# Optimization experiments

Hardware: AMD Instinct MI355X
Metric: run time of the kernel (lower is better)

Reference implementation:

```python
import jax, jax.numpy as jnp
import numpy as np

B, T, C, H = 2, 2048, 1024, 16
DH = C // H  # 64


def setup_inputs() -> dict:
    key = jax.random.key(0)
    ks = jax.random.split(key, 8)
    scale = 1.0 / np.sqrt(C)
    x = jax.random.normal(ks[0], (B, T, C), dtype=jnp.float32)
    mask = jax.random.randint(ks[1], (B, T), 0, 2, dtype=jnp.int32)
    Wq = jax.random.normal(ks[2], (C, C), dtype=jnp.float32) * scale
    bq = jnp.zeros((C,), dtype=jnp.float32)
    Wk = jax.random.normal(ks[3], (C, C), dtype=jnp.float32) * scale
    bk = jnp.zeros((C,), dtype=jnp.float32)
    Wv = jax.random.normal(ks[4], (C, C), dtype=jnp.float32) * scale
    bv = jnp.zeros((C,), dtype=jnp.float32)
    return {"x": x, "Wq": Wq, "bq": bq, "Wk": Wk, "bk": bk, "Wv": Wv, "bv": bv, "mask": mask}


def reference(x, Wq, bq, Wk, bk, Wv, bv, mask):
    # q/k/v projections: [B,T,C] -> [B,H,T,DH]
    def proj(W, b):
        return (x @ W + b).reshape(B, T, H, DH).transpose(0, 2, 1, 3)

    q = proj(Wq, bq)
    k = proj(Wk, bk)
    v = proj(Wv, bv)

    att = jnp.einsum("bhqd,bhkd->bhqk", q, k) * (1.0 / np.sqrt(DH))

    # outer-product padding mask: square_mask[b,q,k] = mask[b,q]*mask[b,k]
    m = mask.astype(jnp.float32)
    square_mask = m[:, :, None] * m[:, None, :]           # [B,T,T]
    sm = (square_mask != 0)[:, None, :, :]                 # [B,1,T,T]
    att = jnp.where(sm, att, -jnp.inf)

    # rows that are fully masked (query token padded) -> softmax gives NaN
    # in torch; torch then zeros the NaNs. Replicate with a safe softmax.
    row_valid = (mask != 0)[:, None, :, None]              # [B,1,T,1]
    att_safe = jnp.where(row_valid, att, 0.0)
    att = jax.nn.softmax(att_safe, axis=-1)
    att = jnp.where(row_valid, att, 0.0)
    # attn_pdrop = 0.0 -> dropout is identity

    y = jnp.einsum("bhqk,bhkd->bhqd", att, v)              # [B,H,T,DH]
    y = y.transpose(0, 2, 1, 3).reshape(B, T, C)
    return y
```

## Files before the change

### kernel.cpp

```cpp
#include <hip/hip_runtime.h>

#define B_ 2
#define T_ 2048
#define C_ 1024
#define H_ 16
#define DH_ 64

typedef __attribute__((ext_vector_type(8))) _Float16 half8;
typedef __attribute__((ext_vector_type(4))) _Float16 half4;
typedef __attribute__((ext_vector_type(2))) __fp16 fp16x2;
typedef __attribute__((ext_vector_type(4))) float f32x4;
typedef __attribute__((ext_vector_type(16))) float f32x16;

__device__ __forceinline__ unsigned short f2h(float f) {
    union { _Float16 h; unsigned short u; } cv; cv.h = (_Float16)f; return cv.u;
}
__device__ __forceinline__ unsigned pk2(float a, float b) {
    union { fp16x2 h; unsigned u; } cv;
    cv.h = __builtin_amdgcn_cvt_pkrtz(a, b);
    return cv.u;
}
__device__ __forceinline__ void plswap(unsigned &a, unsigned &b) {
    asm volatile("v_permlane32_swap_b32 %0, %1" : "+v"(a), "+v"(b));
}

__device__ __forceinline__ void gll16(const void* g, void* l) {
    __builtin_amdgcn_global_load_lds(
        (const __attribute__((address_space(1))) void*)g,
        (__attribute__((address_space(3))) void*)l, 16, 0, 0);
}

__global__ __launch_bounds__(256) void prep_kernel(
    const float* __restrict__ x, unsigned short* __restrict__ xf,
    const int* __restrict__ mask, unsigned short* __restrict__ mb,
    const float* __restrict__ Wq, const float* __restrict__ Wk,
    const float* __restrict__ Wv, unsigned short* __restrict__ wt)
{
    __shared__ float tile[32][33];
    const int tid = threadIdx.x;

    if (blockIdx.x < 2048) {
        const size_t idx8 = ((size_t)blockIdx.x * 256 + tid) * 8;
        float4 v0 = *(const float4*)(x + idx8);
        float4 v1 = *(const float4*)(x + idx8 + 4);
        float f[8] = {v0.x, v0.y, v0.z, v0.w, v1.x, v1.y, v1.z, v1.w};
        unsigned short h[8];
#pragma unroll
        for (int i = 0; i < 8; i++) h[i] = f2h(f[i]);
        *(uint4*)(xf + idx8) = *(const uint4*)h;

        if (blockIdx.x == 0) {
#pragma unroll
            for (int j = 0; j < 16; j++) {
                int i = tid * 16 + j;
                mb[i] = (mask[i] != 0) ? (unsigned short)0x3C00 : (unsigned short)0;
            }
        }
    } else {
        const int idx = blockIdx.x - 2048;
        const int z   = idx >> 10;
        const int rem = idx & 1023;
        const int n0  = (rem & 31) * 32;
        const int k0  = (rem >> 5) * 32;
        const float* __restrict__ W = (z == 0) ? Wq : (z == 1) ? Wk : Wv;
        unsigned short* __restrict__ wtz = wt + (size_t)z * C_ * C_;
        const int tx = tid & 31;
        const int ty = tid >> 5;
#pragma unroll
        for (int j = 0; j < 4; j++)
            tile[ty + j * 8][tx] = W[(size_t)(k0 + ty + j * 8) * C_ + n0 + tx];
        __syncthreads();
#pragma unroll
        for (int j = 0; j < 4; j++)
            wtz[(size_t)(n0 + ty + j * 8) * C_ + k0 + tx] = f2h(tile[tx][ty + j * 8]);
    }
}

__global__ __launch_bounds__(256) void qkv_mfma_kernel(
    const unsigned short* __restrict__ xf, const unsigned short* __restrict__ wt,
    const float* __restrict__ bq, const float* __restrict__ bk,
    const float* __restrict__ bv, const int* __restrict__ maskp,
    unsigned short* __restrict__ qb, unsigned short* __restrict__ kb,
    unsigned short* __restrict__ vt)
{
    __shared__ unsigned short sX[128 * 64];
    __shared__ unsigned short sW[128 * 64];

    const int z = blockIdx.z;
    const float* __restrict__ bias = (z == 0) ? bq : (z == 1) ? bk : bv;
    const unsigned short* __restrict__ wtz = wt + (size_t)z * C_ * C_;

    const int tok0 = blockIdx.x * 128;
    const int col0 = blockIdx.y * 128;
    const int wv    = threadIdx.x >> 6;
    const int lane  = threadIdx.x & 63;
    const int l15   = lane & 15;
    const int quad  = lane >> 4;
    const int l7    = l15 & 7;
    const int wm    = wv >> 1;
    const int wn    = wv & 1;
    const int lrow8 = lane >> 3;
    const int gch   = (lane & 7) ^ lrow8;

    f32x4 acc[4][4];
#pragma unroll
    for (int i = 0; i < 4; i++)
#pragma unroll
        for (int j = 0; j < 4; j++) acc[i][j] = (f32x4){0.f, 0.f, 0.f, 0.f};

    int aoff[4][2], boff[4][2];
#pragma unroll
    for (int i = 0; i < 4; i++)
#pragma unroll
        for (int s = 0; s < 2; s++) {
            aoff[i][s] = (wm * 64 + i * 16 + l15) * 64 + (((s * 4 + quad) ^ l7) * 8);
            boff[i][s] = (wn * 64 + i * 16 + l15) * 64 + (((s * 4 + quad) ^ l7) * 8);
        }

    const unsigned short* Abuf = (z < 2) ? sX : sW;
    const unsigned short* Bbuf = (z < 2) ? sW : sX;

    for (int k0 = 0; k0 < C_; k0 += 64) {
        __syncthreads();
#pragma unroll
        for (int s = 0; s < 8; ++s) {
            int g    = (s << 2) + wv;
            int tsel = g >> 4;
            int r0   = (g & 15) << 3;
            const unsigned short* src = tsel ? wtz : xf;
            unsigned short*       dst = tsel ? sW  : sX;
            int rowg = tsel ? col0 : tok0;
            gll16(src + (size_t)(rowg + r0 + lrow8) * C_ + k0 + gch * 8,
                  dst + r0 * 64);
        }
        __syncthreads();

        half8 af[4][2], bf_[4][2];
#pragma unroll
        for (int i = 0; i < 4; i++)
#pragma unroll
            for (int s = 0; s < 2; s++) {
                af[i][s]  = *(const half8*)&Abuf[aoff[i][s]];
                bf_[i][s] = *(const half8*)&Bbuf[boff[i][s]];
            }
#pragma unroll
        for (int s = 0; s < 2; s++)
#pragma unroll
            for (int j = 0; j < 4; j++)
#pragma unroll
                for (int i = 0; i < 4; i++)
                    acc[i][j] = __builtin_amdgcn_mfma_f32_16x16x32_f16(
                        af[i][s], bf_[j][s], acc[i][j], 0, 0, 0);
    }

    if (z == 0) {
#pragma unroll
        for (int j = 0; j < 4; j++) {
            int col = col0 + wn * 64 + j * 16 + l15;
            int h = col >> 6, d = col & 63;
            float bs = bias[col];
#pragma unroll
            for (int i = 0; i < 4; i++) {
#pragma unroll
                for (int r = 0; r < 4; r++) {
                    int tok = tok0 + wm * 64 + i * 16 + quad * 4 + r;
                    int bidx = tok >> 11, t = tok & (T_ - 1);
                    qb[((size_t)(bidx * H_ + h) * T_ + t) * DH_ + d] =
                        f2h((acc[i][j][r] + bs) * 0.18033688011112042f);
                }
            }
        }
    } else if (z == 1) {
#pragma unroll
        for (int j = 0; j < 4; j++) {
            int col = col0 + wn * 64 + j * 16 + l15;
            int h = col >> 6, d = col & 63;
            float bs = bias[col];
#pragma unroll
            for (int i = 0; i < 4; i++) {
#pragma unroll
                for (int r = 0; r < 4; r++) {
                    int tok = tok0 + wm * 64 + i * 16 + quad * 4 + r;
                    int bidx = tok >> 11, t = tok & (T_ - 1);
                    kb[((size_t)(bidx * H_ + h) * T_ + t) * DH_ + d] =
                        f2h(acc[i][j][r] + bs);
                }
            }
        }
    } else {
        float mv4[4]; int bidx4[4], t4[4];
#pragma unroll
        for (int j = 0; j < 4; j++) {
            int tok = tok0 + wn * 64 + j * 16 + l15;
            bidx4[j] = tok >> 11; t4[j] = tok & (T_ - 1);
            mv4[j] = (maskp[bidx4[j] * T_ + t4[j]] != 0) ? 1.f : 0.f;
        }
#pragma unroll
        for (int i = 0; i < 4; i++) {
#pragma unroll
            for (int r = 0; r < 4; r++) {
                int col = col0 + wm * 64 + i * 16 + quad * 4 + r;
                int h = col >> 6, d = col & 63;
                float bs = bias[col];
#pragma unroll
                for (int j = 0; j < 4; j++) {
                    vt[((size_t)(bidx4[j] * H_ + h) * DH_ + d) * T_ + t4[j]] =
                        f2h((acc[i][j][r] + bs) * mv4[j]);
                }
            }
        }
    }
}

__global__ __launch_bounds__(256, 2) void attn_mfma_kernel(
    const unsigned short* __restrict__ qb,
    const unsigned short* __restrict__ kb,
    const unsigned short* __restrict__ vt,
    const int* __restrict__ mask,
    const unsigned short* __restrict__ mb,
    float* __restrict__ out)
{
    __shared__ unsigned short Ks[2][64 * 64];
    __shared__ unsigned short Vs[2][64 * 64];

    const int bh   = blockIdx.x;
    const int b    = bh >> 4;
    const int h    = bh & 15;
    const int wv   = threadIdx.x >> 6;
    const int lane = threadIdx.x & 63;
    const int l31  = lane & 31;
    const int hi   = lane >> 5;
    const int l7b  = l31 & 7;
    const int q0w  = blockIdx.y * 128 + wv * 32;

    const unsigned short* kbh = kb + (size_t)bh * T_ * DH_;
    const unsigned short* vbh = vt + (size_t)bh * DH_ * T_;
    const unsigned short* mbb = mb + b * T_;
    const int* __restrict__ mrow = mask + b * T_;

    half8 qf[4];
#pragma unroll
    for (int m = 0; m < 4; ++m)
        qf[m] = *(const half8*)(qb + ((size_t)bh * T_ + q0w + l31) * DH_
                                + m * 16 + hi * 8);

    f32x16 o0, o1, lacc;
#pragma unroll
    for (int r = 0; r < 16; ++r) { o0[r] = 0.f; o1[r] = 0.f; lacc[r] = 0.f; }

    const int lrow = lane >> 3;
    const int gch  = (lane & 7) ^ lrow;

#pragma unroll
    for (int s = 0; s < 4; ++s) {
        int j  = (wv << 2) + s;
        int rb = j & 7;
        if (j < 8) gll16(kbh + (size_t)(rb * 8 + lrow) * DH_ + gch * 8, &Ks[0][rb * 512]);
        else       gll16(vbh + (size_t)(rb * 8 + lrow) * T_  + gch * 8, &Vs[0][rb * 512]);
    }

    for (int kt = 0; kt < 32; ++kt) {
        const int cur   = kt & 1;
        const int kbase = kt * 64;
        __syncthreads();

        if (kt < 31) {
            const int nb = kbase + 64;
#pragma unroll
            for (int s = 0; s < 4; ++s) {
                int j  = (wv << 2) + s;
                int rb = j & 7;
                if (j < 8) gll16(kbh + (size_t)(nb + rb * 8 + lrow) * DH_ + gch * 8,
                                 &Ks[cur ^ 1][rb * 512]);
                else       gll16(vbh + (size_t)(rb * 8 + lrow) * T_ + nb + gch * 8,
                                 &Vs[cur ^ 1][rb * 512]);
            }
        }

        const unsigned short* Kc = &Ks[cur][0];
        const unsigned short* Vc = &Vs[cur][0];

        half8 bm[4];
#pragma unroll
        for (int c = 0; c < 4; ++c)
            bm[c] = *(const half8*)(mbb + kbase + c * 16 + hi * 8);

        half8 pa[4];
#pragma unroll
        for (int st = 0; st < 2; ++st) {
            f32x16 sa;
#pragma unroll
            for (int r = 0; r < 16; ++r) sa[r] = 0.f;
#pragma unroll
            for (int m = 0; m < 4; ++m) {
                half8 kf = *(const half8*)(Kc + (st * 32 + l31) * 64
                                           + (((m * 2 + hi) ^ l7b) * 8));
                sa = __builtin_amdgcn_mfma_f32_32x32x16_f16(kf, qf[m], sa, 0, 0, 0);
            }
            float p[16];
#pragma unroll
            for (int r = 0; r < 16; ++r) p[r] = __builtin_amdgcn_exp2f(sa[r]);
#pragma unroll
            for (int kh = 0; kh < 2; ++kh) {
                unsigned w0 = pk2(p[kh * 8 + 0], p[kh * 8 + 1]);
                unsigned w2 = pk2(p[kh * 8 + 4], p[kh * 8 + 5]);
                unsigned w1 = pk2(p[kh * 8 + 2], p[kh * 8 + 3]);
                unsigned w3 = pk2(p[kh * 8 + 6], p[kh * 8 + 7]);
                plswap(w0, w2);
                plswap(w1, w3);
                union { unsigned u[4]; half8 hh; } cv;
                cv.u[0] = w0; cv.u[1] = w1; cv.u[2] = w2; cv.u[3] = w3;
                pa[st * 2 + kh] = cv.hh;
            }
        }

#pragma unroll
        for (int c = 0; c < 4; ++c)
            lacc = __builtin_amdgcn_mfma_f32_32x32x16_f16(pa[c], bm[c], lacc, 0, 0, 0);

#pragma unroll
        for (int c = 0; c < 4; ++c) {
            half8 v0 = *(const half8*)(Vc + (l31) * 64      + (((c * 2 + hi) ^ l7b) * 8));
            half8 v1 = *(const half8*)(Vc + (32 + l31) * 64 + (((c * 2 + hi) ^ l7b) * 8));
            o0 = __builtin_amdgcn_mfma_f32_32x32x16_f16(pa[c], v0, o0, 0, 0, 0);
            o1 = __builtin_amdgcn_mfma_f32_32x32x16_f16(pa[c], v1, o1, 0, 0, 0);
        }
    }

#pragma unroll
    for (int r = 0; r < 16; ++r) {
        int q = q0w + (r & 3) + 8 * (r >> 2) + 4 * hi;
        float lv = lacc[r];
        float iv = (mrow[q] != 0 && lv > 0.f) ? (1.0f / lv) : 0.f;
        float* orow = out + ((size_t)(b * T_ + q)) * C_ + h * DH_;
        orow[l31]      = o0[r] * iv;
        orow[32 + l31] = o1[r] * iv;
    }
}

extern "C" void kernel_launch(void* const* d_in, const int* in_sizes, int n_in,
                              void* d_out, int out_size, void* d_ws, size_t ws_size,
                              hipStream_t stream)
{
    (void)in_sizes; (void)n_in; (void)out_size; (void)ws_size;
    const float* x  = (const float*)d_in[0];
    const float* Wq = (const float*)d_in[1];
    const float* bq = (const float*)d_in[2];
    const float* Wk = (const float*)d_in[3];
    const float* bk = (const float*)d_in[4];
    const float* Wv = (const float*)d_in[5];
    const float* bv = (const float*)d_in[6];
    const int* mask = (const int*)d_in[7];
    float* out = (float*)d_out;

    const size_t NX = (size_t)B_ * T_ * C_;
    unsigned short* xf = (unsigned short*)d_ws;
    unsigned short* wt = xf + NX;
    unsigned short* qb = wt + (size_t)3 * C_ * C_;
    unsigned short* kb = qb + NX;
    unsigned short* vt = kb + NX;
    unsigned short* mb = vt + NX;

    prep_kernel<<<5120, 256, 0, stream>>>(x, xf, mask, mb, Wq, Wk, Wv, wt);
    qkv_mfma_kernel<<<dim3(32, 8, 3), 256, 0, stream>>>(
        xf, wt, bq, bk, bv, mask, qb, kb, vt);
    attn_mfma_kernel<<<dim3(32, 16), 256, 0, stream>>>(qb, kb, vt, mask, mb, out);
}
```

Measured before the change: 167.2 us.

## Split attention key range across two blocks with flag-based partial combine

Splits the key loop into two halves handled by separate blocks (grid z=2), doubling block count from 512 to 1024. The first block to finish writes its unnormalized partial output and row sums to global memory and raises a flag. The second block spins on that flag, then adds the partials and normalizes. This relies on the softmax using no running max, so the partials add directly. It adds global round-trips and a spin-wait, and depends on both blocks making forward progress.

```diff
diff --git a/kernel.cpp b/kernel.cpp
--- a/kernel.cpp
+++ b/kernel.cpp
@@ -34,7 +34,8 @@
     const float* __restrict__ x, unsigned short* __restrict__ xf,
     const int* __restrict__ mask, unsigned short* __restrict__ mb,
     const float* __restrict__ Wq, const float* __restrict__ Wk,
-    const float* __restrict__ Wv, unsigned short* __restrict__ wt)
+    const float* __restrict__ Wv, unsigned short* __restrict__ wt,
+    unsigned* __restrict__ flags)
 {
     __shared__ float tile[32][33];
     const int tid = threadIdx.x;
@@ -55,6 +56,10 @@
                 int i = tid * 16 + j;
                 mb[i] = (mask[i] != 0) ? (unsigned short)0x3C00 : (unsigned short)0;
             }
+        }
+        if (blockIdx.x == 1) {
+            flags[tid] = 0u;
+            flags[tid + 256] = 0u;
         }
     } else {
         const int idx = blockIdx.x - 2048;
@@ -218,14 +223,19 @@
     const unsigned short* __restrict__ vt,
     const int* __restrict__ mask,
     const unsigned short* __restrict__ mb,
-    float* __restrict__ out)
+    float* __restrict__ out,
+    float* __restrict__ lo,
+    unsigned* __restrict__ flags)
 {
     __shared__ unsigned short Ks[2][64 * 64];
     __shared__ unsigned short Vs[2][64 * 64];
+    __shared__ unsigned role_sh;
 
     const int bh   = blockIdx.x;
     const int b    = bh >> 4;
     const int h    = bh & 15;
+    const int ks   = blockIdx.z;
+    const int kb0  = ks << 10;
     const int wv   = threadIdx.x >> 6;
     const int lane = threadIdx.x & 63;
     const int l31  = lane & 31;
@@ -255,16 +265,18 @@
     for (int s = 0; s < 4; ++s) {
         int j  = (wv << 2) + s;
         int rb = j & 7;
-        if (j < 8) gll16(kbh + (size_t)(rb * 8 + lrow) * DH_ + gch * 8, &Ks[0][rb * 512]);
-        else       gll16(vbh + (size_t)(rb * 8 + lrow) * T_  + gch * 8, &Vs[0][rb * 512]);
-    }
-
-    for (int kt = 0; kt < 32; ++kt) {
-        const int cur   = kt & 1;
-        const int kbase = kt * 64;
-        __syncthreads();
-
-        if (kt < 31) {
+        if (j < 8) gll16(kbh + (size_t)(kb0 + rb * 8 + lrow) * DH_ + gch * 8,
+                         &Ks[0][rb * 512]);
+        else       gll16(vbh + (size_t)(rb * 8 + lrow) * T_ + kb0 + gch * 8,
+                         &Vs[0][rb * 512]);
+    }
+
+    for (int ktl = 0; ktl < 16; ++ktl) {
+        const int cur   = ktl & 1;
+        const int kbase = kb0 + ktl * 64;
+        __syncthreads();
+
+        if (ktl < 15) {
             const int nb = kbase + 64;
 #pragma unroll
             for (int s = 0; s < 4; ++s) {
@@ -327,14 +339,44 @@
         }
     }
 
-#pragma unroll
-    for (int r = 0; r < 16; ++r) {
-        int q = q0w + (r & 3) + 8 * (r >> 2) + 4 * hi;
-        float lv = lacc[r];
-        float iv = (mrow[q] != 0 && lv > 0.f) ? (1.0f / lv) : 0.f;
-        float* orow = out + ((size_t)(b * T_ + q)) * C_ + h * DH_;
-        orow[l31]      = o0[r] * iv;
-        orow[32 + l31] = o1[r] * iv;
+    const int pidx = bh * 16 + blockIdx.y;
+    if (threadIdx.x == 0)
+        role_sh = __hip_atomic_fetch_add(&flags[pidx], 1u, __ATOMIC_ACQ_REL,
+                                         __HIP_MEMORY_SCOPE_AGENT);
+    __syncthreads();
+    const unsigned role = role_sh;
+
+    if (role == 0) {
+#pragma unroll
+        for (int r = 0; r < 16; ++r) {
+            int q = q0w + (r & 3) + 8 * (r >> 2) + 4 * hi;
+            float* orow = out + ((size_t)(b * T_ + q)) * C_ + h * DH_;
+            orow[l31]      = o0[r];
+            orow[32 + l31] = o1[r];
+            if (l31 == 0) lo[bh * T_ + q] = lacc[r];
+        }
+        __threadfence();
+        __syncthreads();
+        if (threadIdx.x == 0)
+            __hip_atomic_fetch_add(&flags[pidx], 4u, __ATOMIC_RELEASE,
+                                   __HIP_MEMORY_SCOPE_AGENT);
+    } else {
+        if (threadIdx.x == 0) {
+            while (!(__hip_atomic_load(&flags[pidx], __ATOMIC_ACQUIRE,
+                                       __HIP_MEMORY_SCOPE_AGENT) & 4u))
+                __builtin_amdgcn_s_sleep(2);
+        }
+        __syncthreads();
+        __threadfence();
+#pragma unroll
+        for (int r = 0; r < 16; ++r) {
+            int q = q0w + (r & 3) + 8 * (r >> 2) + 4 * hi;
+            float lsum = lacc[r] + lo[bh * T_ + q];
+            float iv = (mrow[q] != 0 && lsum > 0.f) ? (1.0f / lsum) : 0.f;
+            float* orow = out + ((size_t)(b * T_ + q)) * C_ + h * DH_;
+            orow[l31]      = (o0[r] + orow[l31])      * iv;
+            orow[32 + l31] = (o1[r] + orow[32 + l31]) * iv;
+        }
     }
 }
 
@@ -360,9 +402,12 @@
     unsigned short* kb = qb + NX;
     unsigned short* vt = kb + NX;
     unsigned short* mb = vt + NX;
-
-    prep_kernel<<<5120, 256, 0, stream>>>(x, xf, mask, mb, Wq, Wk, Wv, wt);
+    float* lo          = (float*)(mb + 4096);
+    unsigned* flags    = (unsigned*)(lo + 32 * T_);
+
+    prep_kernel<<<5120, 256, 0, stream>>>(x, xf, mask, mb, Wq, Wk, Wv, wt, flags);
     qkv_mfma_kernel<<<dim3(32, 8, 3), 256, 0, stream>>>(
         xf, wt, bq, bk, bv, mask, qb, kb, vt);
-    attn_mfma_kernel<<<dim3(32, 16), 256, 0, stream>>>(qb, kb, vt, mask, mb, out);
-}
+    attn_mfma_kernel<<<dim3(32, 16, 2), 256, 0, stream>>>(
+        qb, kb, vt, mask, mb, out, lo, flags);
+}
```

Measured after the change: 310.6 us. 1.86x slower.
